# Optimization experiments

Measured on AMD Instinct MI355X. Metric: run time of the kernel, lower is better.

## Reference

```python
import jax, jax.numpy as jnp
import numpy as np

EPS = 1e-5

def setup_inputs() -> dict:
    key = jax.random.key(0)
    k0, k1 = jax.random.split(key, 2)
    N6, M5, M4 = 524288, 131072, 32768
    Cin, Cout = 256, 512
    data = jax.random.normal(k0, (N6, Cin), dtype=jnp.float32)
    weight = jax.random.normal(k1, (Cout, Cin), dtype=jnp.float32) * (1.0 / np.sqrt(Cin))
    gamma = jnp.ones((Cout,), dtype=jnp.float32)
    beta = jnp.zeros((Cout,), dtype=jnp.float32)
    # indices of non-empty nodes at the coarser depth (sorted, unique):
    # depth 6 has N6/8 = 65536 parents among M5 = 131072 depth-5 nodes (stride 2)
    idx5 = (jnp.arange(N6 // 8, dtype=jnp.int32) * (M5 // (N6 // 8)))
    # depth 5 has M5/8 = 16384 parents among M4 = 32768 depth-4 nodes (stride 2)
    idx4 = (jnp.arange(M5 // 8, dtype=jnp.int32) * (M4 // (M5 // 8)))
    return {"data": data, "weight": weight, "gamma": gamma, "beta": beta,
            "idx5": idx5, "idx4": idx4, "nnum5": M5, "nnum4": M4,
            "in_depth": 6, "out_depth": 4}

def _octree_max_pool(x, idx, nnum):
    # x: [N, C] child features in sibling groups of 8 -> pooled [N/8, C],
    # scattered (octree_pad) into the full coarser level of size nnum.
    N, C = x.shape
    y = x.reshape(N // 8, 8, C).max(axis=1)
    return jnp.zeros((nnum, C), x.dtype).at[idx].set(y)

def reference(data, weight, gamma, beta, idx5, idx4, nnum5, nnum4, in_depth, out_depth):
    out = data
    # in_depth (6) > out_depth (4): pool twice, then conv1x1+BN+ReLU
    for idx, nnum in ((idx5, nnum5), (idx4, nnum4)):
        out = _octree_max_pool(out, idx, nnum)
    h = out @ weight.T                      # 1x1 conv == bias-free linear
    mean = h.mean(axis=0)
    var = h.var(axis=0)
    h = (h - mean) * jax.lax.rsqrt(var + EPS) * gamma + beta
    return jax.nn.relu(h)
```

## Files before the change

kernel.cpp:

```cpp
#include <hip/hip_runtime.h>
#include <hip/hip_bf16.h>
#include <math.h>

#define CIN 256
#define COUT 512

typedef __attribute__((ext_vector_type(8))) short bf16x8;
typedef __attribute__((ext_vector_type(4))) float f32x4;
typedef __attribute__((ext_vector_type(4))) float f32x4v;

__device__ __forceinline__ ushort f2bf(float f) {
    union { float f; unsigned u; } x; x.f = f;
    unsigned r = x.u + 0x7FFFu + ((x.u >> 16) & 1u);
    return (ushort)(r >> 16);
}
__device__ __forceinline__ float bf2f(ushort u) {
    union { unsigned u; float f; } x; x.u = (unsigned)u << 16; return x.f;
}

__device__ __forceinline__ int lbound(const int* __restrict__ a, int n, int key) {
    int lo = 0, hi = n;
    while (lo < hi) {
        int m = (lo + hi) >> 1;
        if (a[m] < key) lo = m + 1; else hi = m;
    }
    return lo;
}

__global__ __launch_bounds__(256) void pool_prep_kernel(const float* __restrict__ data,
                                                        const int* __restrict__ idx5, int n_i5,
                                                        const int* __restrict__ idx4, int n_i4,
                                                        const float* __restrict__ W,
                                                        ushort* __restrict__ Wb,
                                                        ushort* __restrict__ P, int G2,
                                                        int* __restrict__ inv4, int n4) {
    const int b = blockIdx.x;
    const int nPool = G2 >> 2;
    const int t = threadIdx.x;

    if (b >= nPool) {
        int rb = b - nPool;
        if (rb < 32) {
            int q0 = rb * 1024 + t;
            #pragma unroll
            for (int j = 0; j < 4; ++j) {
                int i = (q0 + j * 256) * 4;
                float4 v = *reinterpret_cast<const float4*>(W + i);
                ushort4 o;
                o.x = f2bf(v.x); o.y = f2bf(v.y); o.z = f2bf(v.z); o.w = f2bf(v.w);
                *reinterpret_cast<ushort4*>(&Wb[i]) = o;
            }
        } else {
            int i = (rb - 32) * 256 + t;
            if (i < n_i4) {
                int s = idx4[i];
                inv4[s] = i;
                int e = (i + 1 < n_i4) ? idx4[i + 1] : n4;
                for (int k = s + 1; k < e; ++k) inv4[k] = -1;
                if (i == 0) for (int k = 0; k < s; ++k) inv4[k] = -1;
            }
        }
        return;
    }

    __shared__ int lb[5];
    if (t < 5) lb[t] = lbound(idx5, n_i5, b * 32 + t * 8);
    __syncthreads();

    const int w = t >> 6, lane = t & 63;
    int lo  = __builtin_amdgcn_readfirstlane(lb[w]);
    int cnt = __builtin_amdgcn_readfirstlane(lb[w + 1]) - lo;

    float4 acc = make_float4(-INFINITY, -INFINITY, -INFINITY, -INFINITY);
    const float* base = data + (size_t)lo * (8 * CIN) + lane * 4;
    #pragma unroll
    for (int j = 0; j < 8; ++j) {
        if (j < cnt) {
            #pragma unroll
            for (int r = 0; r < 8; ++r) {
                f32x4v v = __builtin_nontemporal_load(
                    reinterpret_cast<const f32x4v*>(base + ((size_t)j * 8 + r) * CIN));
                acc.x = fmaxf(acc.x, v.x);
                acc.y = fmaxf(acc.y, v.y);
                acc.z = fmaxf(acc.z, v.z);
                acc.w = fmaxf(acc.w, v.w);
            }
        }
    }
    if (cnt < 8) {
        acc.x = fmaxf(acc.x, 0.f);
        acc.y = fmaxf(acc.y, 0.f);
        acc.z = fmaxf(acc.z, 0.f);
        acc.w = fmaxf(acc.w, 0.f);
    }
    ushort4 o;
    o.x = f2bf(acc.x); o.y = f2bf(acc.y); o.z = f2bf(acc.z); o.w = f2bf(acc.w);
    *reinterpret_cast<ushort4*>(&P[(size_t)(b * 4 + w) * CIN + lane * 4]) = o;
}

__global__ __launch_bounds__(256) void mfma_gemm_kernel(const ushort* __restrict__ A,
                                                        const ushort* __restrict__ B,
                                                        ushort* __restrict__ H,
                                                        float* __restrict__ partial) {
    __shared__ __align__(16) ushort Asm[128 * 64];
    __shared__ __align__(16) ushort Bsm[128 * 64];

    int t = threadIdx.x;
    int lane = t & 63;
    int wid = t >> 6;
    int wm = wid >> 1, wn = wid & 1;
    int m0 = blockIdx.x * 128, n0 = blockIdx.y * 128;

    f32x4 acc[4][4] = {};

    for (int k0 = 0; k0 < CIN; k0 += 64) {
        #pragma unroll
        for (int i = 0; i < 4; ++i) {
            int idx = i * 256 + t;
            int row = idx >> 3;
            int sl  = idx & 7;
            bf16x8 av = *reinterpret_cast<const bf16x8*>(A + (size_t)(m0 + row) * CIN + k0 + sl * 8);
            bf16x8 bv = *reinterpret_cast<const bf16x8*>(B + (size_t)(n0 + row) * CIN + k0 + sl * 8);
            int ws = (sl ^ (row & 7)) * 8;
            *reinterpret_cast<bf16x8*>(&Asm[row * 64 + ws]) = av;
            *reinterpret_cast<bf16x8*>(&Bsm[row * 64 + ws]) = bv;
        }
        __syncthreads();

        #pragma unroll
        for (int ks = 0; ks < 2; ++ks) {
            bf16x8 af[4], bfr[4];
            int slog = ks * 4 + (lane >> 4);
            #pragma unroll
            for (int mi = 0; mi < 4; ++mi) {
                int row = wm * 64 + mi * 16 + (lane & 15);
                af[mi] = *reinterpret_cast<const bf16x8*>(&Asm[row * 64 + (slog ^ (row & 7)) * 8]);
            }
            #pragma unroll
            for (int ni = 0; ni < 4; ++ni) {
                int col = wn * 64 + ni * 16 + (lane & 15);
                bfr[ni] = *reinterpret_cast<const bf16x8*>(&Bsm[col * 64 + (slog ^ (col & 7)) * 8]);
            }
            #pragma unroll
            for (int mi = 0; mi < 4; ++mi)
                #pragma unroll
                for (int ni = 0; ni < 4; ++ni)
                    acc[mi][ni] = __builtin_amdgcn_mfma_f32_16x16x32_bf16(af[mi], bfr[ni], acc[mi][ni], 0, 0, 0);
        }
        __syncthreads();
    }

    float s[4], q[4];
    #pragma unroll
    for (int ni = 0; ni < 4; ++ni) {
        s[ni] = 0.f; q[ni] = 0.f;
        #pragma unroll
        for (int mi = 0; mi < 4; ++mi)
            #pragma unroll
            for (int r = 0; r < 4; ++r) {
                float v = acc[mi][ni][r];
                s[ni] += v;
                q[ni] = fmaf(v, v, q[ni]);
            }
        s[ni] += __shfl_xor(s[ni], 16); s[ni] += __shfl_xor(s[ni], 32);
        q[ni] += __shfl_xor(q[ni], 16); q[ni] += __shfl_xor(q[ni], 32);
    }
    float* redS = (float*)Asm;
    float* redQ = redS + 256;
    if (lane < 16) {
        #pragma unroll
        for (int ni = 0; ni < 4; ++ni) {
            int c = wn * 64 + ni * 16 + lane;
            redS[wm * 128 + c] = s[ni];
            redQ[wm * 128 + c] = q[ni];
        }
    }
    __syncthreads();
    if (t < 128) {
        float S = redS[t] + redS[128 + t];
        float Q = redQ[t] + redQ[128 + t];
        partial[(size_t)blockIdx.x * 1024 + blockIdx.y * 128 + t]       = S;
        partial[(size_t)blockIdx.x * 1024 + 512 + blockIdx.y * 128 + t] = Q;
    }

    #pragma unroll
    for (int mi = 0; mi < 4; ++mi) {
        #pragma unroll
        for (int ni = 0; ni < 4; ++ni) {
            int col   = n0 + wn * 64 + ni * 16 + (lane & 15);
            int rbase = m0 + wm * 64 + mi * 16 + (lane >> 4) * 4;
            #pragma unroll
            for (int r = 0; r < 4; ++r)
                H[(size_t)(rbase + r) * COUT + col] = f2bf(acc[mi][ni][r]);
        }
    }
}

__global__ __launch_bounds__(128) void bn_finalize_kernel(const float* __restrict__ partial,
                                                          const float* __restrict__ gamma,
                                                          const float* __restrict__ beta,
                                                          float* __restrict__ scale,
                                                          float* __restrict__ shift,
                                                          float invN) {
    __shared__ float sS[2], sQ[2];
    int c = blockIdx.x;
    int p = threadIdx.x;
    float S = partial[(size_t)p * 1024 + c];
    float Q = partial[(size_t)p * 1024 + 512 + c];
    #pragma unroll
    for (int off = 1; off < 64; off <<= 1) {
        S += __shfl_xor(S, off);
        Q += __shfl_xor(Q, off);
    }
    int lane = p & 63, w = p >> 6;
    if (lane == 0) { sS[w] = S; sQ[w] = Q; }
    __syncthreads();
    if (p == 0) {
        float Sf = sS[0] + sS[1];
        float Qf = sQ[0] + sQ[1];
        float mean = Sf * invN;
        float var  = fmaf(Qf, invN, -mean * mean);
        float inv  = rsqrtf(var + 1e-5f);
        float sc   = gamma[c] * inv;
        scale[c] = sc;
        shift[c] = fmaf(-mean, sc, beta[c]);
    }
}

__global__ __launch_bounds__(256) void out_kernel(const ushort* __restrict__ H,
                                                  const int* __restrict__ inv4,
                                                  const float* __restrict__ scale,
                                                  const float* __restrict__ shift,
                                                  float* __restrict__ out, int rows) {
    __shared__ float scl[512], sht[512];
    int t = threadIdx.x;
    scl[t]       = scale[t];
    scl[t + 256] = scale[t + 256];
    sht[t]       = shift[t];
    sht[t + 256] = shift[t + 256];
    __syncthreads();

    int r = blockIdx.x * 32 + (t >> 3);
    if (r >= rows) return;
    int c0 = (t & 7) * 8;
    int j = inv4[r];
    float* orow = out + (size_t)r * COUT;

    if (j >= 0) {
        const ushort* hrow = H + (size_t)j * COUT;
        #pragma unroll
        for (int i = 0; i < 8; ++i) {
            int c = c0 + i * 64;
            bf16x8 h = *reinterpret_cast<const bf16x8*>(hrow + c);
            float4 a, b;
            a.x = fmaxf(fmaf(bf2f((ushort)h[0]), scl[c + 0], sht[c + 0]), 0.f);
            a.y = fmaxf(fmaf(bf2f((ushort)h[1]), scl[c + 1], sht[c + 1]), 0.f);
            a.z = fmaxf(fmaf(bf2f((ushort)h[2]), scl[c + 2], sht[c + 2]), 0.f);
            a.w = fmaxf(fmaf(bf2f((ushort)h[3]), scl[c + 3], sht[c + 3]), 0.f);
            b.x = fmaxf(fmaf(bf2f((ushort)h[4]), scl[c + 4], sht[c + 4]), 0.f);
            b.y = fmaxf(fmaf(bf2f((ushort)h[5]), scl[c + 5], sht[c + 5]), 0.f);
            b.z = fmaxf(fmaf(bf2f((ushort)h[6]), scl[c + 6], sht[c + 6]), 0.f);
            b.w = fmaxf(fmaf(bf2f((ushort)h[7]), scl[c + 7], sht[c + 7]), 0.f);
            *reinterpret_cast<float4*>(orow + c)     = a;
            *reinterpret_cast<float4*>(orow + c + 4) = b;
        }
    } else {
        #pragma unroll
        for (int i = 0; i < 8; ++i) {
            int c = c0 + i * 64;
            float4 a, b;
            a.x = fmaxf(sht[c + 0], 0.f);
            a.y = fmaxf(sht[c + 1], 0.f);
            a.z = fmaxf(sht[c + 2], 0.f);
            a.w = fmaxf(sht[c + 3], 0.f);
            b.x = fmaxf(sht[c + 4], 0.f);
            b.y = fmaxf(sht[c + 5], 0.f);
            b.z = fmaxf(sht[c + 6], 0.f);
            b.w = fmaxf(sht[c + 7], 0.f);
            *reinterpret_cast<float4*>(orow + c)     = a;
            *reinterpret_cast<float4*>(orow + c + 4) = b;
        }
    }
}

extern "C" void kernel_launch(void* const* d_in, const int* in_sizes, int n_in,
                              void* d_out, int out_size, void* d_ws, size_t ws_size,
                              hipStream_t stream) {
    const float* data   = (const float*)d_in[0];
    const float* weight = (const float*)d_in[1];
    const float* gamma  = (const float*)d_in[2];
    const float* beta   = (const float*)d_in[3];
    const int*   idx5   = (const int*)d_in[4];
    const int*   idx4   = (const int*)d_in[5];

    const int n_i5 = in_sizes[4];
    const int n_i4 = in_sizes[5];
    const int G2   = n_i4;
    const int rows = out_size / COUT;
    const int M    = G2;
    const int MB   = M / 128;

    char* w = (char*)d_ws;
    ushort* P      = (ushort*)w;                        w += (size_t)G2 * CIN * sizeof(ushort);
    ushort* H      = (ushort*)w;                        w += (size_t)G2 * COUT * sizeof(ushort);
    ushort* Wb     = (ushort*)w;                        w += (size_t)COUT * CIN * sizeof(ushort);
    float* partial = (float*)w;                         w += (size_t)MB * 1024 * sizeof(float);
    float* scale   = (float*)w;                         w += COUT * sizeof(float);
    float* shift   = (float*)w;                         w += COUT * sizeof(float);
    int*   inv4    = (int*)w;                           w += (size_t)rows * sizeof(int);

    pool_prep_kernel<<<G2 / 4 + 32 + (n_i4 + 255) / 256, 256, 0, stream>>>(
        data, idx5, n_i5, idx4, n_i4, weight, Wb, P, G2, inv4, rows);

    {
        dim3 grid(MB, COUT / 128);
        mfma_gemm_kernel<<<grid, 256, 0, stream>>>(P, Wb, H, partial);
    }
    bn_finalize_kernel<<<COUT, 128, 0, stream>>>(partial, gamma, beta, scale, shift,
                                                 1.0f / (float)rows);
    out_kernel<<<(rows + 31) / 32, 256, 0, stream>>>(H, inv4, scale, shift,
                                                     (float*)d_out, rows);
}
```

Measured before the change: 129.6 us.

## Stage full-K A tile in LDS once and stream weights directly from global

The GEMM kernel now loads the whole 128x256 bf16 A tile into LDS with a single barrier and reads B fragments straight from global memory, removing the per-K-step LDS staging and barrier pairs. The pool-prep kernel block order is also reshuffled so the weight-conversion and inverse-index blocks come first, with the inverse-index block count hardcoded to 64. Exchange: 64KB of LDS per block lowers occupancy, and B fragment loads from global/L2 are uncoalesced-ish and unhidden. The hardcoded 64 blocks only cover n_i4 up to 16384, which matches the current input size.

```diff
diff --git a/kernel.cpp b/kernel.cpp
--- a/kernel.cpp
+++ b/kernel.cpp
@@ -35,36 +35,35 @@
                                                         ushort* __restrict__ P, int G2,
                                                         int* __restrict__ inv4, int n4) {
     const int b = blockIdx.x;
-    const int nPool = G2 >> 2;
     const int t = threadIdx.x;
 
-    if (b >= nPool) {
-        int rb = b - nPool;
-        if (rb < 32) {
-            int q0 = rb * 1024 + t;
-            #pragma unroll
-            for (int j = 0; j < 4; ++j) {
-                int i = (q0 + j * 256) * 4;
-                float4 v = *reinterpret_cast<const float4*>(W + i);
-                ushort4 o;
-                o.x = f2bf(v.x); o.y = f2bf(v.y); o.z = f2bf(v.z); o.w = f2bf(v.w);
-                *reinterpret_cast<ushort4*>(&Wb[i]) = o;
-            }
-        } else {
-            int i = (rb - 32) * 256 + t;
-            if (i < n_i4) {
-                int s = idx4[i];
-                inv4[s] = i;
-                int e = (i + 1 < n_i4) ? idx4[i + 1] : n4;
-                for (int k = s + 1; k < e; ++k) inv4[k] = -1;
-                if (i == 0) for (int k = 0; k < s; ++k) inv4[k] = -1;
-            }
+    if (b < 32) {
+        int q0 = b * 1024 + t;
+        #pragma unroll
+        for (int j = 0; j < 4; ++j) {
+            int i = (q0 + j * 256) * 4;
+            float4 v = *reinterpret_cast<const float4*>(W + i);
+            ushort4 o;
+            o.x = f2bf(v.x); o.y = f2bf(v.y); o.z = f2bf(v.z); o.w = f2bf(v.w);
+            *reinterpret_cast<ushort4*>(&Wb[i]) = o;
         }
         return;
     }
-
+    if (b < 96) {
+        int i = (b - 32) * 256 + t;
+        if (i < n_i4) {
+            int s = idx4[i];
+            inv4[s] = i;
+            int e = (i + 1 < n_i4) ? idx4[i + 1] : n4;
+            for (int k = s + 1; k < e; ++k) inv4[k] = -1;
+            if (i == 0) for (int k = 0; k < s; ++k) inv4[k] = -1;
+        }
+        return;
+    }
+
+    const int pb = b - 96;
     __shared__ int lb[5];
-    if (t < 5) lb[t] = lbound(idx5, n_i5, b * 32 + t * 8);
+    if (t < 5) lb[t] = lbound(idx5, n_i5, pb * 32 + t * 8);
     __syncthreads();
 
     const int w = t >> 6, lane = t & 63;
@@ -95,15 +94,14 @@
     }
     ushort4 o;
     o.x = f2bf(acc.x); o.y = f2bf(acc.y); o.z = f2bf(acc.z); o.w = f2bf(acc.w);
-    *reinterpret_cast<ushort4*>(&P[(size_t)(b * 4 + w) * CIN + lane * 4]) = o;
-}
-
-__global__ __launch_bounds__(256) void mfma_gemm_kernel(const ushort* __restrict__ A,
-                                                        const ushort* __restrict__ B,
+    *reinterpret_cast<ushort4*>(&P[(size_t)(pb * 4 + w) * CIN + lane * 4]) = o;
+}
+
+__global__ __launch_bounds__(256) void mfma_gemm_kernel(const ushort* __restrict__ P,
+                                                        const ushort* __restrict__ Wb,
                                                         ushort* __restrict__ H,
                                                         float* __restrict__ partial) {
-    __shared__ __align__(16) ushort Asm[128 * 64];
-    __shared__ __align__(16) ushort Bsm[128 * 64];
+    __shared__ __align__(16) ushort Asm[128 * 256];
 
     int t = threadIdx.x;
     int lane = t & 63;
@@ -111,43 +109,37 @@
     int wm = wid >> 1, wn = wid & 1;
     int m0 = blockIdx.x * 128, n0 = blockIdx.y * 128;
 
+    #pragma unroll
+    for (int i = 0; i < 16; ++i) {
+        int idx = i * 256 + t;
+        int row = idx >> 5;
+        int ch  = idx & 31;
+        bf16x8 v = *reinterpret_cast<const bf16x8*>(P + (size_t)(m0 + row) * CIN + ch * 8);
+        *reinterpret_cast<bf16x8*>(&Asm[row * 256 + ((ch ^ (row & 31)) << 3)]) = v;
+    }
+    __syncthreads();
+
     f32x4 acc[4][4] = {};
-
-    for (int k0 = 0; k0 < CIN; k0 += 64) {
-        #pragma unroll
-        for (int i = 0; i < 4; ++i) {
-            int idx = i * 256 + t;
-            int row = idx >> 3;
-            int sl  = idx & 7;
-            bf16x8 av = *reinterpret_cast<const bf16x8*>(A + (size_t)(m0 + row) * CIN + k0 + sl * 8);
-            bf16x8 bv = *reinterpret_cast<const bf16x8*>(B + (size_t)(n0 + row) * CIN + k0 + sl * 8);
-            int ws = (sl ^ (row & 7)) * 8;
-            *reinterpret_cast<bf16x8*>(&Asm[row * 64 + ws]) = av;
-            *reinterpret_cast<bf16x8*>(&Bsm[row * 64 + ws]) = bv;
-        }
-        __syncthreads();
-
-        #pragma unroll
-        for (int ks = 0; ks < 2; ++ks) {
-            bf16x8 af[4], bfr[4];
-            int slog = ks * 4 + (lane >> 4);
+    #pragma unroll
+    for (int st = 0; st < 8; ++st) {
+        bf16x8 af[4], bfr[4];
+        #pragma unroll
+        for (int ni = 0; ni < 4; ++ni) {
+            int col = n0 + wn * 64 + ni * 16 + (lane & 15);
+            bfr[ni] = *reinterpret_cast<const bf16x8*>(
+                Wb + (size_t)col * CIN + st * 32 + (lane >> 4) * 8);
+        }
+        #pragma unroll
+        for (int mi = 0; mi < 4; ++mi) {
+            int row = wm * 64 + mi * 16 + (lane & 15);
+            int lc  = st * 4 + (lane >> 4);
+            af[mi] = *reinterpret_cast<const bf16x8*>(&Asm[row * 256 + ((lc ^ (row & 31)) << 3)]);
+        }
+        #pragma unroll
+        for (int mi = 0; mi < 4; ++mi)
             #pragma unroll
-            for (int mi = 0; mi < 4; ++mi) {
-                int row = wm * 64 + mi * 16 + (lane & 15);
-                af[mi] = *reinterpret_cast<const bf16x8*>(&Asm[row * 64 + (slog ^ (row & 7)) * 8]);
-            }
-            #pragma unroll
-            for (int ni = 0; ni < 4; ++ni) {
-                int col = wn * 64 + ni * 16 + (lane & 15);
-                bfr[ni] = *reinterpret_cast<const bf16x8*>(&Bsm[col * 64 + (slog ^ (col & 7)) * 8]);
-            }
-            #pragma unroll
-            for (int mi = 0; mi < 4; ++mi)
-                #pragma unroll
-                for (int ni = 0; ni < 4; ++ni)
-                    acc[mi][ni] = __builtin_amdgcn_mfma_f32_16x16x32_bf16(af[mi], bfr[ni], acc[mi][ni], 0, 0, 0);
-        }
-        __syncthreads();
+            for (int ni = 0; ni < 4; ++ni)
+                acc[mi][ni] = __builtin_amdgcn_mfma_f32_16x16x32_bf16(af[mi], bfr[ni], acc[mi][ni], 0, 0, 0);
     }
 
     float s[4], q[4];
@@ -165,6 +157,7 @@
         s[ni] += __shfl_xor(s[ni], 16); s[ni] += __shfl_xor(s[ni], 32);
         q[ni] += __shfl_xor(q[ni], 16); q[ni] += __shfl_xor(q[ni], 32);
     }
+    __syncthreads();
     float* redS = (float*)Asm;
     float* redQ = redS + 256;
     if (lane < 16) {
@@ -309,7 +302,7 @@
     float* shift   = (float*)w;                         w += COUT * sizeof(float);
     int*   inv4    = (int*)w;                           w += (size_t)rows * sizeof(int);
 
-    pool_prep_kernel<<<G2 / 4 + 32 + (n_i4 + 255) / 256, 256, 0, stream>>>(
+    pool_prep_kernel<<<96 + G2 / 4, 256, 0, stream>>>(
         data, idx5, n_i5, idx4, n_i4, weight, Wb, P, G2, inv4, rows);
 
     {
```

Result: slower. 134.1 us (+3.5%).
